# Optimization experiments

Hardware: AMD Instinct MI355X
Metric: run time of the kernel (lower is better)

Reference implementation:

```python
import jax, jax.numpy as jnp
import numpy as np

B, S, D, H, HD = 2, 2048, 2048, 16, 128

def _freqs_cis(dim, end, theta=10000.0):
    freqs = 1.0 / theta ** (np.arange(0, dim, 2, dtype=np.float32)[: dim // 2] / dim)
    t = np.arange(end, dtype=np.float32)
    f = np.outer(t, freqs).astype(np.float32)
    f = np.concatenate((f, f), axis=-1)
    return jnp.asarray(np.cos(f)), jnp.asarray(np.sin(f))

def _rotate_half(x):
    x1, x2 = x[..., : x.shape[-1] // 2], x[..., x.shape[-1] // 2 :]
    return jnp.concatenate((-x2, x1), axis=-1)

def setup_inputs() -> dict:
    key = jax.random.key(0)
    ks = jax.random.split(key, 5)
    x = jax.random.normal(ks[0], (B, S, D), jnp.float32)
    scale = 1.0 / np.sqrt(D)
    Wq = jax.random.normal(ks[1], (D, H, HD), jnp.float32) * scale
    Wk = jax.random.normal(ks[2], (D, H, HD), jnp.float32) * scale
    Wv = jax.random.normal(ks[3], (D, H, HD), jnp.float32) * scale
    Wo = jax.random.normal(ks[4], (H, HD, D), jnp.float32) * (1.0 / np.sqrt(D))
    mask = jnp.tril(jnp.ones((S, S), jnp.bool_))[None, None]  # causal [1,1,S,S]
    return {"x": x, "mask": mask, "Wq": Wq, "Wk": Wk, "Wv": Wv, "Wo": Wo}

def reference(x, mask, Wq, Wk, Wv, Wo):
    # QKV projections: [B,S,D] -> [B,S,H,HD]
    q = jnp.einsum('bsd,dhk->bshk', x, Wq)
    k = jnp.einsum('bsd,dhk->bshk', x, Wk)
    v = jnp.einsum('bsd,dhk->bshk', x, Wv)
    # RoPE
    cos, sin = _freqs_cis(HD, x.shape[1])
    cos = cos[None, :, None, :]
    sin = sin[None, :, None, :]
    q = q * cos + _rotate_half(q) * sin
    k = k * cos + _rotate_half(k) * sin
    # scaled dot-product attention
    scores = jnp.einsum('bqhk,bshk->bhqs', q, k) / jnp.sqrt(jnp.asarray(HD, q.dtype))
    big_neg = jnp.finfo(scores.dtype).min
    scores = jnp.where(mask, scores, big_neg)
    attn = jax.nn.softmax(scores, axis=-1)
    ctx = jnp.einsum('bhqs,bshk->bqhk', attn, v)
    # output projection contracting (heads, head_dim)
    return jnp.einsum('bqhk,hkd->bqd', ctx, Wo)
```

## Files before the change

kernel.cpp:

```cpp
#include <hip/hip_runtime.h>

typedef unsigned short u16;
typedef unsigned int u32;

constexpr int Bc = 2, Sc = 2048, Dc = 2048, Hc = 16, HDc = 128;

using short8 = __attribute__((ext_vector_type(8))) short;
using f32x4v = __attribute__((ext_vector_type(4))) float;

static __device__ __forceinline__ float bf2f(u16 v) { return __uint_as_float(((u32)v) << 16); }
static __device__ __forceinline__ u16 f2bf(float f) {
    u32 u = __float_as_uint(f);
    return (u16)((u + 0x7fffu + ((u >> 16) & 1u)) >> 16);
}

__device__ __forceinline__ void gll16(const u16* g, u16* l) {
    __builtin_amdgcn_global_load_lds((const __attribute__((address_space(1))) void*)g,
                                     (__attribute__((address_space(3))) void*)l, 16, 0, 0);
}

__global__ __launch_bounds__(256) void rope_tab_k(float* __restrict__ ctab, float* __restrict__ stab) {
    int idx = blockIdx.x * 256 + threadIdx.x;
    int s = idx >> 6, i = idx & 63;
    float freq = exp2f(-(float)i * 0.20762050593045952f);
    float ang = (float)s * freq;
    float c, sn;
    sincosf(ang, &sn, &c);
    ctab[idx] = c;
    stab[idx] = sn;
}

__global__ __launch_bounds__(256) void cvt_k(const float* __restrict__ in, u16* __restrict__ out, int n) {
    int i = (blockIdx.x * 256 + threadIdx.x) * 8;
    if (i >= n) return;
    float4 a = *(const float4*)(in + i);
    float4 b = *(const float4*)(in + i + 4);
    u16 r[8] = {f2bf(a.x), f2bf(a.y), f2bf(a.z), f2bf(a.w),
                f2bf(b.x), f2bf(b.y), f2bf(b.z), f2bf(b.w)};
    *(uint4*)(out + i) = *(uint4*)r;
}

__global__ __launch_bounds__(256) void tcvt3_k(const float* __restrict__ in0, const float* __restrict__ in1,
                                               const float* __restrict__ in2, u16* __restrict__ out,
                                               int R, int C) {
    __shared__ u16 tile[64][68];
    const float* in = (blockIdx.z == 0) ? in0 : (blockIdx.z == 1) ? in1 : in2;
    u16* o = out + (size_t)blockIdx.z * R * C;
    int bx = blockIdx.x * 64, by = blockIdx.y * 64;
    int t = threadIdx.x;
    int r = t >> 4, c4 = (t & 15) * 4;
    #pragma unroll
    for (int i = 0; i < 4; ++i) {
        int row = by + r + i * 16;
        float4 v = *(const float4*)(in + (size_t)row * C + bx + c4);
        u16* d = &tile[r + i * 16][c4];
        d[0] = f2bf(v.x); d[1] = f2bf(v.y); d[2] = f2bf(v.z); d[3] = f2bf(v.w);
    }
    __syncthreads();
    int oc = t >> 4, r4 = (t & 15) * 4;
    #pragma unroll
    for (int i = 0; i < 4; ++i) {
        int orow = oc + i * 16;
        u16 v[4] = {tile[r4][orow], tile[r4 + 1][orow], tile[r4 + 2][orow], tile[r4 + 3][orow]};
        *(uint2*)&o[(size_t)(bx + orow) * R + by + r4] = *(const uint2*)v;
    }
}

template <int MODE>
__global__ __launch_bounds__(256) void gemm_bt(const u16* __restrict__ A, const u16* __restrict__ Bt,
                                               float* __restrict__ C2,
                                               int M, int N, int K) {
    __shared__ u16 SM[8192];
    u16* As = SM;
    u16* Bs = SM + 4096;
    int m0 = blockIdx.y * 128, n0 = blockIdx.x * 128;
    int t = threadIdx.x;
    int wid = t >> 6, lane = t & 63;
    int wr = wid >> 1, wc = wid & 1;
    f32x4v acc[4][4] = {};

    int c0 = wid * 128 + lane;
    int c1 = wid * 128 + 64 + lane;
    const u16* Ar0 = A + (size_t)(m0 + (c0 >> 2)) * K + (((c0 & 3) ^ ((c0 >> 3) & 3)) * 8);
    const u16* Ar1 = A + (size_t)(m0 + (c1 >> 2)) * K + (((c1 & 3) ^ ((c1 >> 3) & 3)) * 8);
    const u16* Br0 = Bt + (size_t)(n0 + (c0 >> 2)) * K + (((c0 & 3) ^ ((c0 >> 3) & 3)) * 8);
    const u16* Br1 = Bt + (size_t)(n0 + (c1 >> 2)) * K + (((c1 & 3) ^ ((c1 >> 3) & 3)) * 8);
    u16* Al0 = As + (size_t)(wid * 128) * 8;
    u16* Al1 = As + (size_t)(wid * 128 + 64) * 8;
    u16* Bl0 = Bs + (size_t)(wid * 128) * 8;
    u16* Bl1 = Bs + (size_t)(wid * 128 + 64) * 8;

    int sw = (lane >> 1) & 3;
    const u16* ap = As + (wr * 64 + (lane & 15)) * 32 + ((((lane >> 4)) ^ sw) << 3);
    const u16* bp = Bs + (wc * 64 + (lane & 15)) * 32 + ((((lane >> 4)) ^ sw) << 3);

    for (int kk = 0; kk < K; kk += 32) {
        gll16(Ar0 + kk, Al0);
        gll16(Ar1 + kk, Al1);
        gll16(Br0 + kk, Bl0);
        gll16(Br1 + kk, Bl1);
        __syncthreads();
        short8 a[4], b[4];
        #pragma unroll
        for (int i = 0; i < 4; ++i) {
            a[i] = *(const short8*)(ap + i * 512);
            b[i] = *(const short8*)(bp + i * 512);
        }
        #pragma unroll
        for (int mf = 0; mf < 4; ++mf)
            #pragma unroll
            for (int nf = 0; nf < 4; ++nf)
                acc[mf][nf] = __builtin_amdgcn_mfma_f32_16x16x32_bf16(a[mf], b[nf], acc[mf][nf], 0, 0, 0);
        __syncthreads();
    }

    int ln = lane & 15, lq = lane >> 4;
    int rb = m0 + wr * 64 + (lq << 2);
    int cb = n0 + wc * 64 + ln;
    #pragma unroll
    for (int mf = 0; mf < 4; ++mf)
        #pragma unroll
        for (int nf = 0; nf < 4; ++nf)
            #pragma unroll
            for (int r = 0; r < 4; ++r)
                C2[(size_t)(rb + mf * 16 + r) * N + cb + nf * 16] = acc[mf][nf][r];
}


#define FENCE asm volatile("" ::: "memory")

#define RDA8(P) do { _Pragma("unroll") for (int m_ = 0; m_ < 4; ++m_) { \
    aF[m_][0] = *(const short8*)((P) + m_ * 1024 + co0); \
    aF[m_][1] = *(const short8*)((P) + m_ * 1024 + co1); } } while (0)

#define RDB2(P, nh) do { _Pragma("unroll") for (int j_ = 0; j_ < 2; ++j_) { \
    bF[j_][0] = *(const short8*)((P) + ((nh) * 2 + j_) * 1024 + co0); \
    bF[j_][1] = *(const short8*)((P) + ((nh) * 2 + j_) * 1024 + co1); } } while (0)

#define MFQ8(nh) do { _Pragma("unroll") for (int m_ = 0; m_ < 4; ++m_) \
    _Pragma("unroll") for (int j_ = 0; j_ < 2; ++j_) { \
    f32x4v& c_ = acc[m_][(nh) * 2 + j_]; \
    c_ = __builtin_amdgcn_mfma_f32_16x16x32_bf16(aF[m_][0], bF[j_][0], c_, 0, 0, 0); \
    c_ = __builtin_amdgcn_mfma_f32_16x16x32_bf16(aF[m_][1], bF[j_][1], c_, 0, 0, 0); } } while (0)

#define PT(nh) do { FENCE; __builtin_amdgcn_s_barrier(); FENCE; \
    asm volatile("s_waitcnt lgkmcnt(0)" ::: "memory"); \
    __builtin_amdgcn_s_setprio(1); MFQ8(nh); __builtin_amdgcn_s_setprio(0); \
    FENCE; __builtin_amdgcn_s_barrier(); FENCE; } while (0)

#define KTILE(aRb, bRb, KST, ADST, BDST, VW) do { \
    RDA8(aRb); RDB2(bRb, 0); \
    if ((KST) >= 0) stageA(KST, ADST); \
    PT(0); \
    RDB2(bRb, 1); \
    if ((KST) >= 0) stageB(KST, BDST); \
    if ((VW) == 6) asm volatile("s_waitcnt vmcnt(6)" ::: "memory"); \
    else if ((VW) == 0) asm volatile("s_waitcnt vmcnt(0)" ::: "memory"); \
    PT(1); } while (0)

__global__ __launch_bounds__(512, 2) void gemm128_qkv(
        const u16* __restrict__ A, const u16* __restrict__ Bt,
        u16* __restrict__ Oq, u16* __restrict__ Ok, u16* __restrict__ Ov,
        const float* __restrict__ ctab, const float* __restrict__ stab) {
    __shared__ u16 SM[73728];
    constexpr int K = Dc;
    constexpr int NT = 32;
    int t = threadIdx.x, wid = t >> 6, lane = t & 63;
    int wm = wid >> 2, wn = wid & 3;
    int ln = lane & 15, lq = lane >> 4;

    int nx = gridDim.x;
    int lin = blockIdx.y * nx + blockIdx.x;
    int cpx = (nx * gridDim.y) >> 3;
    int swzb = (lin & 7) * cpx + (lin >> 3);
    int n0 = (swzb % nx) << 8;
    int m0 = (swzb / nx) << 7;

    u16* As0 = SM;
    u16* As1 = SM + 8192;
    u16* As2 = SM + 16384;
    u16* Bs0 = SM + 24576;
    u16* Bs1 = SM + 40960;
    u16* Bs2 = SM + 57344;

    auto stageA = [&](int kt, u16* dst) {
        #pragma unroll
        for (int L = 0; L < 2; ++L) {
            int ch16 = L * 512 + wid * 64 + lane;
            int row = ch16 >> 3, ch = ch16 & 7;
            gll16(A + (size_t)(m0 + row) * K + kt * 64 + ((ch ^ (row & 7)) << 3),
                  dst + (L * 512 + wid * 64) * 8);
        }
    };
    auto stageB = [&](int kt, u16* dst) {
        #pragma unroll
        for (int L = 0; L < 4; ++L) {
            int ch16 = L * 512 + wid * 64 + lane;
            int row = ch16 >> 3, ch = ch16 & 7;
            gll16(Bt + (size_t)(n0 + row) * K + kt * 64 + ((ch ^ (row & 7)) << 3),
                  dst + (L * 512 + wid * 64) * 8);
        }
    };

    const u16* aR0 = As0 + (wm * 64 + ln) * 64;
    const u16* aR1 = As1 + (wm * 64 + ln) * 64;
    const u16* aR2 = As2 + (wm * 64 + ln) * 64;
    const u16* bR0 = Bs0 + (wn * 64 + ln) * 64;
    const u16* bR1 = Bs1 + (wn * 64 + ln) * 64;
    const u16* bR2 = Bs2 + (wn * 64 + ln) * 64;
    int sw = ln & 7;
    int co0 = (lq ^ sw) << 3;
    int co1 = ((4 | lq) ^ sw) << 3;

    short8 aF[4][2], bF[2][2];
    f32x4v acc[4][4] = {};

    stageA(0, As0); stageB(0, Bs0);
    stageA(1, As1); stageB(1, Bs1);
    asm volatile("s_waitcnt vmcnt(6)" ::: "memory");
    FENCE; __builtin_amdgcn_s_barrier(); FENCE;

    for (int k3 = 0; k3 < NT - 2; k3 += 3) {
        KTILE(aR0, bR0, k3 + 2, As2, Bs2, 6);
        KTILE(aR1, bR1, k3 + 3, As0, Bs0, 6);
        KTILE(aR2, bR2, k3 + 4, As1, Bs1, 6);
    }
    KTILE(aR0, bR0, -1, As0, Bs0, 0);
    KTILE(aR1, bR1, -1, As0, Bs0, -1);

    asm volatile("s_waitcnt vmcnt(0)" ::: "memory");
    __syncthreads();

    int which = n0 >> 11;
    int h0 = (n0 & 2047) >> 7;
    int b_ = m0 >> 11;
    int s0 = m0 & (Sc - 1);
    u16* Es = SM;
    const int ESTR = 258;

    #pragma unroll
    for (int mf = 0; mf < 4; ++mf)
        #pragma unroll
        for (int nf = 0; nf < 4; ++nf)
            #pragma unroll
            for (int r = 0; r < 4; ++r)
                Es[(wm * 64 + mf * 16 + (lq << 2) + r) * ESTR + wn * 64 + nf * 16 + ln] =
                    f2bf(acc[mf][nf][r]);
    __syncthreads();

    if (which < 2) {
        u16* dst0 = which ? Ok : Oq;
        int u = t >> 1, h2 = t & 1;
        int r = u & 127, hh = u >> 7;
        int s = s0 + r;
        const u16* rowp = Es + r * ESTR + hh * 128;
        const float* ct = ctab + (size_t)s * 64;
        const float* st = stab + (size_t)s * 64;
        u16* dp = dst0 + (((size_t)(b_ * Hc + h0 + hh)) * Sc + s) * HDc + h2 * 64;
        #pragma unroll
        for (int j8 = 0; j8 < 64; j8 += 8) {
            uint4 aa = *(const uint4*)(rowp + j8);
            uint4 bb = *(const uint4*)(rowp + 64 + j8);
            const u16* ap8 = (const u16*)&aa;
            const u16* bp8 = (const u16*)&bb;
            float4 c0f = *(const float4*)(ct + j8);
            float4 c1f = *(const float4*)(ct + j8 + 4);
            float4 sn0 = *(const float4*)(st + j8);
            float4 sn1 = *(const float4*)(st + j8 + 4);
            float cc[8] = {c0f.x, c0f.y, c0f.z, c0f.w, c1f.x, c1f.y, c1f.z, c1f.w};
            float ss[8] = {sn0.x, sn0.y, sn0.z, sn0.w, sn1.x, sn1.y, sn1.z, sn1.w};
            u16 ov[8];
            #pragma unroll
            for (int e = 0; e < 8; ++e) {
                float x1 = bf2f(ap8[e]), x2 = bf2f(bp8[e]);
                ov[e] = h2 ? f2bf(x2 * cc[e] + x1 * ss[e]) : f2bf(x1 * cc[e] - x2 * ss[e]);
            }
            *(uint4*)(dp + j8) = *(const uint4*)ov;
        }
    } else {
        int u = t >> 1, sh = t & 1;
        int d = u & 127, hh = u >> 7;
        u16* dp = Ov + (((size_t)(b_ * Hc + h0 + hh)) * HDc + d) * Sc + s0 + sh * 64;
        #pragma unroll
        for (int r8 = 0; r8 < 64; r8 += 8) {
            u16 ov[8];
            #pragma unroll
            for (int e = 0; e < 8; ++e)
                ov[e] = Es[(sh * 64 + r8 + e) * ESTR + hh * 128 + d];
            *(uint4*)(dp + r8) = *(const uint4*)ov;
        }
    }
}

__global__ __launch_bounds__(256) void fattn_k(const u16* __restrict__ Q, const u16* __restrict__ K,
                                               const u16* __restrict__ Vt, u16* __restrict__ ctx) {
    __shared__ u16 KsA[8192];
    __shared__ u16 VsA[8192];
    __shared__ u16 PsA[4 * 32 * 72];
    int t = threadIdx.x, wid = t >> 6, lane = t & 63;
    int bh = blockIdx.x;
    int yt = blockIdx.y;
    int qi = (yt < 8) ? yt : 23 - yt;
    int q0 = qi << 7;
    int wrow0 = q0 + wid * 32;
    const u16* Qb = Q + ((size_t)bh * Sc + wrow0) * HDc;
    const u16* Kb = K + (size_t)bh * Sc * HDc;
    const u16* Vb = Vt + (size_t)bh * HDc * Sc;
    int ln = lane & 15, lq = lane >> 4;
    u16* psw = PsA + wid * 32 * 72;

    short8 aq[2][4];
    #pragma unroll
    for (int mf = 0; mf < 2; ++mf)
        #pragma unroll
        for (int ks = 0; ks < 4; ++ks)
            aq[mf][ks] = *(const short8*)(Qb + (size_t)(mf * 16 + ln) * HDc + ks * 32 + lq * 8);

    short8 onesb;
    {
        short v = (ln == 0) ? (short)0x3F80 : (short)0;
        #pragma unroll
        for (int e = 0; e < 8; ++e) onesb[e] = v;
    }

    f32x4v o[2][8] = {};
    f32x4v lacc[2] = {};

    const float sc = 0.08838834764831845f;
    const float SHIFT = 12.0f;
    int jendw = wrow0 + 31;
    int jendb = q0 + 127;
    int swz = (ln >> 1) & 3;

    for (int j0 = 0; j0 <= jendb; j0 += 64) {
        #pragma unroll
        for (int i = 0; i < 4; ++i) {
            int p = (wid * 4 + i) * 64 + lane;
            int plane = p >> 8, key = (p >> 2) & 63;
            int qc = (p & 3) ^ ((key >> 1) & 3);
            gll16(Kb + (size_t)(j0 + key) * HDc + plane * 32 + qc * 8,
                  KsA + (size_t)(wid * 4 + i) * 512);
        }
        #pragma unroll
        for (int i = 0; i < 4; ++i) {
            int p = (wid * 4 + i) * 64 + lane;
            int plane = p >> 9, d = (p >> 2) & 127;
            int qc = (p & 3) ^ ((d >> 1) & 3);
            gll16(Vb + (size_t)d * Sc + j0 + plane * 32 + qc * 8,
                  VsA + (size_t)(wid * 4 + i) * 512);
        }
        __syncthreads();

        if (j0 <= jendw) {
            f32x4v sf[2][4] = {};
            #pragma unroll
            for (int ks = 0; ks < 4; ++ks)
                #pragma unroll
                for (int nf = 0; nf < 4; ++nf) {
                    short8 bk = *(const short8*)(KsA + ks * 2048 + (nf * 16 + ln) * 32 + ((lq ^ swz) << 3));
                    sf[0][nf] = __builtin_amdgcn_mfma_f32_16x16x32_bf16(aq[0][ks], bk, sf[0][nf], 0, 0, 0);
                    sf[1][nf] = __builtin_amdgcn_mfma_f32_16x16x32_bf16(aq[1][ks], bk, sf[1][nf], 0, 0, 0);
                }

            bool diag = (j0 + 63 > wrow0);
            #pragma unroll
            for (int mf = 0; mf < 2; ++mf) {
                int rowb = mf * 16 + (lq << 2);
                #pragma unroll
                for (int nf = 0; nf < 4; ++nf) {
                    int col = nf * 16 + ln;
                    int ck = col >> 3, cl = col & 7;
                    #pragma unroll
                    for (int r = 0; r < 4; ++r) {
                        float p = __expf(fmaf(sf[mf][nf][r], sc, -SHIFT));
                        if (diag && (j0 + col > wrow0 + rowb + r)) p = 0.f;
                        int row = rowb + r;
                        psw[row * 72 + ((ck ^ (row & 7)) << 3) + cl] = f2bf(p);
                    }
                }
            }

            short8 ap0[2][2];
            #pragma unroll
            for (int mf = 0; mf < 2; ++mf)
                #pragma unroll
                for (int ks = 0; ks < 2; ++ks)
                    ap0[mf][ks] = *(const short8*)(psw + (mf * 16 + ln) * 72 + (((ks * 4 + lq) ^ (ln & 7)) << 3));
            #pragma unroll
            for (int ks = 0; ks < 2; ++ks) {
                lacc[0] = __builtin_amdgcn_mfma_f32_16x16x32_bf16(ap0[0][ks], onesb, lacc[0], 0, 0, 0);
                lacc[1] = __builtin_amdgcn_mfma_f32_16x16x32_bf16(ap0[1][ks], onesb, lacc[1], 0, 0, 0);
                #pragma unroll
                for (int nd = 0; nd < 8; ++nd) {
                    short8 bv = *(const short8*)(VsA + ks * 4096 + (nd * 16 + ln) * 32 + ((lq ^ swz) << 3));
                    o[0][nd] = __builtin_amdgcn_mfma_f32_16x16x32_bf16(ap0[0][ks], bv, o[0][nd], 0, 0, 0);
                    o[1][nd] = __builtin_amdgcn_mfma_f32_16x16x32_bf16(ap0[1][ks], bv, o[1][nd], 0, 0, 0);
                }
            }
        }
        __syncthreads();
    }

    int b = bh >> 4, h = bh & 15;
    #pragma unroll
    for (int mf = 0; mf < 2; ++mf)
        #pragma unroll
        for (int r = 0; r < 4; ++r) {
            float lv = __shfl(lacc[mf][r], lane & 48, 64);
            float inv = 1.0f / lv;
            int q = wrow0 + mf * 16 + (lq << 2) + r;
            u16* cp = ctx + (((size_t)(b * Sc + q)) * Hc + h) * HDc + ln;
            #pragma unroll
            for (int nd = 0; nd < 8; ++nd)
                cp[nd * 16] = f2bf(o[mf][nd][r] * inv);
        }
}

extern "C" void kernel_launch(void* const* d_in, const int* in_sizes, int n_in,
                              void* d_out, int out_size, void* d_ws, size_t ws_size,
                              hipStream_t stream) {
    (void)in_sizes; (void)n_in; (void)out_size; (void)ws_size;
    const float* x  = (const float*)d_in[0];
    const float* Wq = (const float*)d_in[2];
    const float* Wk = (const float*)d_in[3];
    const float* Wv = (const float*)d_in[4];
    const float* Wo = (const float*)d_in[5];

    char* w = (char*)d_ws;
    u16* Wt  = (u16*)w; w += (size_t)3 * Dc * Dc * 2;
    u16* Qb  = (u16*)w; w += (size_t)Bc * Hc * Sc * HDc * 2;
    u16* Kb  = (u16*)w; w += (size_t)Bc * Hc * Sc * HDc * 2;
    u16* Vb  = (u16*)w; w += (size_t)Bc * Hc * Sc * HDc * 2;
    u16* ctx = (u16*)w; w += (size_t)Bc * Sc * Hc * HDc * 2;
    float* ctab = (float*)w; w += (size_t)Sc * 64 * 4;
    float* stab = (float*)w; w += (size_t)Sc * 64 * 4;
    u16* xb = (u16*)d_out;

    rope_tab_k<<<dim3(Sc * 64 / 256), 256, 0, stream>>>(ctab, stab);

    int nx = Bc * Sc * Dc;
    cvt_k<<<dim3(nx / 2048), 256, 0, stream>>>(x, xb, nx);

    tcvt3_k<<<dim3(Dc / 64, Dc / 64, 3), 256, 0, stream>>>(Wq, Wk, Wv, Wt, Dc, Dc);
    gemm128_qkv<<<dim3(3 * Dc / 256, (Bc * Sc) / 128), 512, 0, stream>>>(
        xb, Wt, Qb, Kb, Vb, ctab, stab);

    fattn_k<<<dim3(Bc * Hc, Sc / 128), 256, 0, stream>>>(Qb, Kb, Vb, ctx);

    tcvt3_k<<<dim3(Dc / 64, Dc / 64, 1), 256, 0, stream>>>(Wo, Wo, Wo, Wt, Dc, Dc);
    gemm_bt<2><<<dim3(Dc / 128, (Bc * Sc) / 128), 256, 0, stream>>>(
        ctx, Wt, (float*)d_out, Bc * Sc, Dc, Dc);
}
```

Before: 424.2 us.

## Swap GEMM pipelines: double-buffered K32 QKV GEMM, triple-buffered output GEMM

The QKV projection GEMM drops the triple-buffered K=64 pipeline and uses a simpler double-buffered K=32 loop with a smaller LDS footprint, so launch bounds allow 4 blocks per CU. The former triple-buffered 128x256 pipeline is reused for the output projection, replacing the simple single-buffered 128x128 gemm_bt with 512-thread blocks. This is meant to raise QKV occupancy and bring latency hiding to the output GEMM. The risk is that the QKV GEMM loses its deeper prefetch and now takes two barriers per 32-wide K step.

```diff
diff --git a/kernel.cpp b/kernel.cpp
--- a/kernel.cpp
+++ b/kernel.cpp
@@ -18,6 +18,8 @@
     __builtin_amdgcn_global_load_lds((const __attribute__((address_space(1))) void*)g,
                                      (__attribute__((address_space(3))) void*)l, 16, 0, 0);
 }
+
+#define FENCE asm volatile("" ::: "memory")
 
 __global__ __launch_bounds__(256) void rope_tab_k(float* __restrict__ ctab, float* __restrict__ stab) {
     int idx = blockIdx.x * 256 + threadIdx.x;
@@ -66,105 +68,12 @@
     }
 }
 
-template <int MODE>
-__global__ __launch_bounds__(256) void gemm_bt(const u16* __restrict__ A, const u16* __restrict__ Bt,
-                                               float* __restrict__ C2,
-                                               int M, int N, int K) {
-    __shared__ u16 SM[8192];
-    u16* As = SM;
-    u16* Bs = SM + 4096;
-    int m0 = blockIdx.y * 128, n0 = blockIdx.x * 128;
-    int t = threadIdx.x;
-    int wid = t >> 6, lane = t & 63;
-    int wr = wid >> 1, wc = wid & 1;
-    f32x4v acc[4][4] = {};
-
-    int c0 = wid * 128 + lane;
-    int c1 = wid * 128 + 64 + lane;
-    const u16* Ar0 = A + (size_t)(m0 + (c0 >> 2)) * K + (((c0 & 3) ^ ((c0 >> 3) & 3)) * 8);
-    const u16* Ar1 = A + (size_t)(m0 + (c1 >> 2)) * K + (((c1 & 3) ^ ((c1 >> 3) & 3)) * 8);
-    const u16* Br0 = Bt + (size_t)(n0 + (c0 >> 2)) * K + (((c0 & 3) ^ ((c0 >> 3) & 3)) * 8);
-    const u16* Br1 = Bt + (size_t)(n0 + (c1 >> 2)) * K + (((c1 & 3) ^ ((c1 >> 3) & 3)) * 8);
-    u16* Al0 = As + (size_t)(wid * 128) * 8;
-    u16* Al1 = As + (size_t)(wid * 128 + 64) * 8;
-    u16* Bl0 = Bs + (size_t)(wid * 128) * 8;
-    u16* Bl1 = Bs + (size_t)(wid * 128 + 64) * 8;
-
-    int sw = (lane >> 1) & 3;
-    const u16* ap = As + (wr * 64 + (lane & 15)) * 32 + ((((lane >> 4)) ^ sw) << 3);
-    const u16* bp = Bs + (wc * 64 + (lane & 15)) * 32 + ((((lane >> 4)) ^ sw) << 3);
-
-    for (int kk = 0; kk < K; kk += 32) {
-        gll16(Ar0 + kk, Al0);
-        gll16(Ar1 + kk, Al1);
-        gll16(Br0 + kk, Bl0);
-        gll16(Br1 + kk, Bl1);
-        __syncthreads();
-        short8 a[4], b[4];
-        #pragma unroll
-        for (int i = 0; i < 4; ++i) {
-            a[i] = *(const short8*)(ap + i * 512);
-            b[i] = *(const short8*)(bp + i * 512);
-        }
-        #pragma unroll
-        for (int mf = 0; mf < 4; ++mf)
-            #pragma unroll
-            for (int nf = 0; nf < 4; ++nf)
-                acc[mf][nf] = __builtin_amdgcn_mfma_f32_16x16x32_bf16(a[mf], b[nf], acc[mf][nf], 0, 0, 0);
-        __syncthreads();
-    }
-
-    int ln = lane & 15, lq = lane >> 4;
-    int rb = m0 + wr * 64 + (lq << 2);
-    int cb = n0 + wc * 64 + ln;
-    #pragma unroll
-    for (int mf = 0; mf < 4; ++mf)
-        #pragma unroll
-        for (int nf = 0; nf < 4; ++nf)
-            #pragma unroll
-            for (int r = 0; r < 4; ++r)
-                C2[(size_t)(rb + mf * 16 + r) * N + cb + nf * 16] = acc[mf][nf][r];
-}
-
-
-#define FENCE asm volatile("" ::: "memory")
-
-#define RDA8(P) do { _Pragma("unroll") for (int m_ = 0; m_ < 4; ++m_) { \
-    aF[m_][0] = *(const short8*)((P) + m_ * 1024 + co0); \
-    aF[m_][1] = *(const short8*)((P) + m_ * 1024 + co1); } } while (0)
-
-#define RDB2(P, nh) do { _Pragma("unroll") for (int j_ = 0; j_ < 2; ++j_) { \
-    bF[j_][0] = *(const short8*)((P) + ((nh) * 2 + j_) * 1024 + co0); \
-    bF[j_][1] = *(const short8*)((P) + ((nh) * 2 + j_) * 1024 + co1); } } while (0)
-
-#define MFQ8(nh) do { _Pragma("unroll") for (int m_ = 0; m_ < 4; ++m_) \
-    _Pragma("unroll") for (int j_ = 0; j_ < 2; ++j_) { \
-    f32x4v& c_ = acc[m_][(nh) * 2 + j_]; \
-    c_ = __builtin_amdgcn_mfma_f32_16x16x32_bf16(aF[m_][0], bF[j_][0], c_, 0, 0, 0); \
-    c_ = __builtin_amdgcn_mfma_f32_16x16x32_bf16(aF[m_][1], bF[j_][1], c_, 0, 0, 0); } } while (0)
-
-#define PT(nh) do { FENCE; __builtin_amdgcn_s_barrier(); FENCE; \
-    asm volatile("s_waitcnt lgkmcnt(0)" ::: "memory"); \
-    __builtin_amdgcn_s_setprio(1); MFQ8(nh); __builtin_amdgcn_s_setprio(0); \
-    FENCE; __builtin_amdgcn_s_barrier(); FENCE; } while (0)
-
-#define KTILE(aRb, bRb, KST, ADST, BDST, VW) do { \
-    RDA8(aRb); RDB2(bRb, 0); \
-    if ((KST) >= 0) stageA(KST, ADST); \
-    PT(0); \
-    RDB2(bRb, 1); \
-    if ((KST) >= 0) stageB(KST, BDST); \
-    if ((VW) == 6) asm volatile("s_waitcnt vmcnt(6)" ::: "memory"); \
-    else if ((VW) == 0) asm volatile("s_waitcnt vmcnt(0)" ::: "memory"); \
-    PT(1); } while (0)
-
-__global__ __launch_bounds__(512, 2) void gemm128_qkv(
+__global__ __launch_bounds__(512, 4) void gemm_qkv32(
         const u16* __restrict__ A, const u16* __restrict__ Bt,
         u16* __restrict__ Oq, u16* __restrict__ Ok, u16* __restrict__ Ov,
         const float* __restrict__ ctab, const float* __restrict__ stab) {
-    __shared__ u16 SM[73728];
+    __shared__ u16 SM[33024];
     constexpr int K = Dc;
-    constexpr int NT = 32;
     int t = threadIdx.x, wid = t >> 6, lane = t & 63;
     int wm = wid >> 2, wn = wid & 3;
     int ln = lane & 15, lq = lane >> 4;
@@ -176,60 +85,54 @@
     int n0 = (swzb % nx) << 8;
     int m0 = (swzb / nx) << 7;
 
-    u16* As0 = SM;
-    u16* As1 = SM + 8192;
-    u16* As2 = SM + 16384;
-    u16* Bs0 = SM + 24576;
-    u16* Bs1 = SM + 40960;
-    u16* Bs2 = SM + 57344;
-
-    auto stageA = [&](int kt, u16* dst) {
+    auto stageAB = [&](int kt, int b) {
+        u16* Ad = SM + b * 12288;
+        u16* Bd = SM + b * 12288 + 4096;
+        {
+            int ci = t;
+            gll16(A + (size_t)(m0 + (ci >> 2)) * K + kt * 32 + (((ci & 3) ^ ((ci >> 3) & 3)) << 3),
+                  Ad + (wid * 64) * 8);
+        }
         #pragma unroll
         for (int L = 0; L < 2; ++L) {
-            int ch16 = L * 512 + wid * 64 + lane;
-            int row = ch16 >> 3, ch = ch16 & 7;
-            gll16(A + (size_t)(m0 + row) * K + kt * 64 + ((ch ^ (row & 7)) << 3),
-                  dst + (L * 512 + wid * 64) * 8);
+            int ci = L * 512 + t;
+            gll16(Bt + (size_t)(n0 + (ci >> 2)) * K + kt * 32 + (((ci & 3) ^ ((ci >> 3) & 3)) << 3),
+                  Bd + (L * 512 + wid * 64) * 8);
         }
     };
-    auto stageB = [&](int kt, u16* dst) {
-        #pragma unroll
-        for (int L = 0; L < 4; ++L) {
-            int ch16 = L * 512 + wid * 64 + lane;
-            int row = ch16 >> 3, ch = ch16 & 7;
-            gll16(Bt + (size_t)(n0 + row) * K + kt * 64 + ((ch ^ (row & 7)) << 3),
-                  dst + (L * 512 + wid * 64) * 8);
-        }
+
+    int co = ((lq ^ ((ln >> 1) & 3)) << 3);
+    f32x4v acc[4][4] = {};
+
+    auto body = [&](const u16* Ab, const u16* Bb) {
+        short8 aF[4], bF[4];
+        #pragma unroll
+        for (int m = 0; m < 4; ++m)
+            aF[m] = *(const short8*)(Ab + (wm * 64 + m * 16 + ln) * 32 + co);
+        #pragma unroll
+        for (int n = 0; n < 4; ++n)
+            bF[n] = *(const short8*)(Bb + (wn * 64 + n * 16 + ln) * 32 + co);
+        __builtin_amdgcn_s_setprio(1);
+        #pragma unroll
+        for (int m = 0; m < 4; ++m)
+            #pragma unroll
+            for (int n = 0; n < 4; ++n)
+                acc[m][n] = __builtin_amdgcn_mfma_f32_16x16x32_bf16(aF[m], bF[n], acc[m][n], 0, 0, 0);
+        __builtin_amdgcn_s_setprio(0);
     };
 
-    const u16* aR0 = As0 + (wm * 64 + ln) * 64;
-    const u16* aR1 = As1 + (wm * 64 + ln) * 64;
-    const u16* aR2 = As2 + (wm * 64 + ln) * 64;
-    const u16* bR0 = Bs0 + (wn * 64 + ln) * 64;
-    const u16* bR1 = Bs1 + (wn * 64 + ln) * 64;
-    const u16* bR2 = Bs2 + (wn * 64 + ln) * 64;
-    int sw = ln & 7;
-    int co0 = (lq ^ sw) << 3;
-    int co1 = ((4 | lq) ^ sw) << 3;
-
-    short8 aF[4][2], bF[2][2];
-    f32x4v acc[4][4] = {};
-
-    stageA(0, As0); stageB(0, Bs0);
-    stageA(1, As1); stageB(1, Bs1);
-    asm volatile("s_waitcnt vmcnt(6)" ::: "memory");
-    FENCE; __builtin_amdgcn_s_barrier(); FENCE;
-
-    for (int k3 = 0; k3 < NT - 2; k3 += 3) {
-        KTILE(aR0, bR0, k3 + 2, As2, Bs2, 6);
-        KTILE(aR1, bR1, k3 + 3, As0, Bs0, 6);
-        KTILE(aR2, bR2, k3 + 4, As1, Bs1, 6);
-    }
-    KTILE(aR0, bR0, -1, As0, Bs0, 0);
-    KTILE(aR1, bR1, -1, As0, Bs0, -1);
-
-    asm volatile("s_waitcnt vmcnt(0)" ::: "memory");
+    stageAB(0, 0);
     __syncthreads();
+
+    #pragma unroll 1
+    for (int kt = 0; kt < 64; kt += 2) {
+        stageAB(kt + 1, 1);
+        body(SM, SM + 4096);
+        __syncthreads();
+        if (kt + 2 < 64) stageAB(kt + 2, 0);
+        body(SM + 12288, SM + 16384);
+        __syncthreads();
+    }
 
     int which = n0 >> 11;
     int h0 = (n0 & 2047) >> 7;
@@ -290,6 +193,116 @@
             *(uint4*)(dp + r8) = *(const uint4*)ov;
         }
     }
+}
+
+
+#define RDA8(P) do { _Pragma("unroll") for (int m_ = 0; m_ < 4; ++m_) { \
+    aF[m_][0] = *(const short8*)((P) + m_ * 1024 + co0); \
+    aF[m_][1] = *(const short8*)((P) + m_ * 1024 + co1); } } while (0)
+
+#define RDB2(P, nh) do { _Pragma("unroll") for (int j_ = 0; j_ < 2; ++j_) { \
+    bF[j_][0] = *(const short8*)((P) + ((nh) * 2 + j_) * 1024 + co0); \
+    bF[j_][1] = *(const short8*)((P) + ((nh) * 2 + j_) * 1024 + co1); } } while (0)
+
+#define MFQ8(nh) do { _Pragma("unroll") for (int m_ = 0; m_ < 4; ++m_) \
+    _Pragma("unroll") for (int j_ = 0; j_ < 2; ++j_) { \
+    f32x4v& c_ = acc[m_][(nh) * 2 + j_]; \
+    c_ = __builtin_amdgcn_mfma_f32_16x16x32_bf16(aF[m_][0], bF[j_][0], c_, 0, 0, 0); \
+    c_ = __builtin_amdgcn_mfma_f32_16x16x32_bf16(aF[m_][1], bF[j_][1], c_, 0, 0, 0); } } while (0)
+
+#define PT(nh) do { FENCE; __builtin_amdgcn_s_barrier(); FENCE; \
+    asm volatile("s_waitcnt lgkmcnt(0)" ::: "memory"); \
+    __builtin_amdgcn_s_setprio(1); MFQ8(nh); __builtin_amdgcn_s_setprio(0); \
+    FENCE; __builtin_amdgcn_s_barrier(); FENCE; } while (0)
+
+#define KTILE(aRb, bRb, KST, ADST, BDST, VW) do { \
+    RDA8(aRb); RDB2(bRb, 0); \
+    if ((KST) >= 0) stageA(KST, ADST); \
+    PT(0); \
+    RDB2(bRb, 1); \
+    if ((KST) >= 0) stageB(KST, BDST); \
+    if ((VW) == 6) asm volatile("s_waitcnt vmcnt(6)" ::: "memory"); \
+    else if ((VW) == 0) asm volatile("s_waitcnt vmcnt(0)" ::: "memory"); \
+    PT(1); } while (0)
+
+__global__ __launch_bounds__(512, 2) void gemm128_op(
+        const u16* __restrict__ A, const u16* __restrict__ Bt, float* __restrict__ C2) {
+    __shared__ u16 SM[73728];
+    constexpr int K = Dc;
+    constexpr int NT = 32;
+    constexpr int N = Dc;
+    int t = threadIdx.x, wid = t >> 6, lane = t & 63;
+    int wm = wid >> 2, wn = wid & 3;
+    int ln = lane & 15, lq = lane >> 4;
+
+    int nx = gridDim.x;
+    int lin = blockIdx.y * nx + blockIdx.x;
+    int cpx = (nx * gridDim.y) >> 3;
+    int swzb = (lin & 7) * cpx + (lin >> 3);
+    int n0 = (swzb % nx) << 8;
+    int m0 = (swzb / nx) << 7;
+
+    u16* As0 = SM;
+    u16* As1 = SM + 8192;
+    u16* As2 = SM + 16384;
+    u16* Bs0 = SM + 24576;
+    u16* Bs1 = SM + 40960;
+    u16* Bs2 = SM + 57344;
+
+    auto stageA = [&](int kt, u16* dst) {
+        #pragma unroll
+        for (int L = 0; L < 2; ++L) {
+            int ch16 = L * 512 + wid * 64 + lane;
+            int row = ch16 >> 3, ch = ch16 & 7;
+            gll16(A + (size_t)(m0 + row) * K + kt * 64 + ((ch ^ (row & 7)) << 3),
+                  dst + (L * 512 + wid * 64) * 8);
+        }
+    };
+    auto stageB = [&](int kt, u16* dst) {
+        #pragma unroll
+        for (int L = 0; L < 4; ++L) {
+            int ch16 = L * 512 + wid * 64 + lane;
+            int row = ch16 >> 3, ch = ch16 & 7;
+            gll16(Bt + (size_t)(n0 + row) * K + kt * 64 + ((ch ^ (row & 7)) << 3),
+                  dst + (L * 512 + wid * 64) * 8);
+        }
+    };
+
+    const u16* aR0 = As0 + (wm * 64 + ln) * 64;
+    const u16* aR1 = As1 + (wm * 64 + ln) * 64;
+    const u16* aR2 = As2 + (wm * 64 + ln) * 64;
+    const u16* bR0 = Bs0 + (wn * 64 + ln) * 64;
+    const u16* bR1 = Bs1 + (wn * 64 + ln) * 64;
+    const u16* bR2 = Bs2 + (wn * 64 + ln) * 64;
+    int sw = ln & 7;
+    int co0 = (lq ^ sw) << 3;
+    int co1 = ((4 | lq) ^ sw) << 3;
+
+    short8 aF[4][2], bF[2][2];
+    f32x4v acc[4][4] = {};
+
+    stageA(0, As0); stageB(0, Bs0);
+    stageA(1, As1); stageB(1, Bs1);
+    asm volatile("s_waitcnt vmcnt(6)" ::: "memory");
+    FENCE; __builtin_amdgcn_s_barrier(); FENCE;
+
+    for (int k3 = 0; k3 < NT - 2; k3 += 3) {
+        KTILE(aR0, bR0, k3 + 2, As2, Bs2, 6);
+        KTILE(aR1, bR1, k3 + 3, As0, Bs0, 6);
+        KTILE(aR2, bR2, k3 + 4, As1, Bs1, 6);
+    }
+    KTILE(aR0, bR0, -1, As0, Bs0, 0);
+    KTILE(aR1, bR1, -1, As0, Bs0, -1);
+
+    int rb = m0 + wm * 64 + (lq << 2);
+    int cb = n0 + wn * 64 + ln;
+    #pragma unroll
+    for (int mf = 0; mf < 4; ++mf)
+        #pragma unroll
+        for (int nf = 0; nf < 4; ++nf)
+            #pragma unroll
+            for (int r = 0; r < 4; ++r)
+                C2[(size_t)(rb + mf * 16 + r) * N + cb + nf * 16] = acc[mf][nf][r];
 }
 
 __global__ __launch_bounds__(256) void fattn_k(const u16* __restrict__ Q, const u16* __restrict__ K,
@@ -442,12 +455,12 @@
     cvt_k<<<dim3(nx / 2048), 256, 0, stream>>>(x, xb, nx);
 
     tcvt3_k<<<dim3(Dc / 64, Dc / 64, 3), 256, 0, stream>>>(Wq, Wk, Wv, Wt, Dc, Dc);
-    gemm128_qkv<<<dim3(3 * Dc / 256, (Bc * Sc) / 128), 512, 0, stream>>>(
+    gemm_qkv32<<<dim3(3 * Dc / 256, (Bc * Sc) / 128), 512, 0, stream>>>(
         xb, Wt, Qb, Kb, Vb, ctab, stab);
 
     fattn_k<<<dim3(Bc * Hc, Sc / 128), 256, 0, stream>>>(Qb, Kb, Vb, ctx);
 
     tcvt3_k<<<dim3(Dc / 64, Dc / 64, 1), 256, 0, stream>>>(Wo, Wo, Wo, Wt, Dc, Dc);
-    gemm_bt<2><<<dim3(Dc / 128, (Bc * Sc) / 128), 256, 0, stream>>>(
-        ctx, Wt, (float*)d_out, Bc * Sc, Dc, Dc);
-}
+    gemm128_op<<<dim3(Dc / 256, (Bc * Sc) / 128), 512, 0, stream>>>(
+        ctx, Wt, (float*)d_out);
+}
```

Measured after the change: 406.1 us. 1.04x faster.
